# Optimization experiments

Hardware: AMD Instinct MI355X
Metric: run time of the kernel (lower is better)

Reference implementation:

```python
import jax, jax.numpy as jnp
import numpy as np

EMBED_DIM = 512
KERNEL = 17


def setup_inputs() -> dict:
    key = jax.random.key(0)
    ks = jax.random.split(key, 5)
    B, L, C = 2, 8192, EMBED_DIM
    s = C ** -0.5
    x = jax.random.normal(ks[0], (B, L, C), dtype=jnp.float32)
    # weights stored as (in, out); equivalent to torch Linear weight.T
    w_qkv = jax.random.normal(ks[1], (C, 3 * C), dtype=jnp.float32) * s
    w_width = jax.random.normal(ks[2], (C, 1), dtype=jnp.float32) * s
    b_width = jax.random.normal(ks[3], (1,), dtype=jnp.float32) * 0.01
    w_out = jax.random.normal(ks[4], (C, C), dtype=jnp.float32) * s
    return {"x": x, "w_qkv": w_qkv, "w_width": w_width, "b_width": b_width, "w_out": w_out}


def reference(x, w_qkv, w_width, b_width, w_out):
    B, L, C = x.shape
    K = KERNEL
    half_k = K // 2
    scale = C ** -0.5

    qkv = x @ w_qkv                      # [B,L,3C]
    q, k, v = jnp.split(qkv, 3, axis=-1)

    # learned soft window width in [1, K]
    width = jax.nn.sigmoid(x @ w_width + b_width) * (K - 1) + 1.0   # [B,L,1]

    # sliding windows of k/v: pad along L then gather K-sized windows
    k_pad = jnp.pad(k, ((0, 0), (half_k, half_k), (0, 0)))
    v_pad = jnp.pad(v, ((0, 0), (half_k, half_k), (0, 0)))
    idx = jnp.arange(L)[:, None] + jnp.arange(K)[None, :]           # [L,K]
    k_win = k_pad[:, idx]                # [B,L,K,C]
    v_win = v_pad[:, idx]                # [B,L,K,C]

    scores = jnp.einsum('blc,blkc->blk', q, k_win) * scale          # [B,L,K]

    rel_pos = jnp.abs(jnp.arange(K, dtype=jnp.float32) - half_k)    # [K]
    soft_mask = jax.nn.sigmoid((width - rel_pos) * 5.0)             # [B,L,K]
    scores = scores - (1.0 - soft_mask) * 10000.0

    attn = jax.nn.softmax(scores, axis=-1)
    out = jnp.einsum('blk,blkc->blc', attn, v_win)                  # [B,L,C]
    return (out + v) @ w_out
```

## Files before the change

kernel.cpp:

```cpp
#include <hip/hip_runtime.h>

typedef unsigned short u16;
typedef unsigned int   u32;
typedef __attribute__((ext_vector_type(8))) short          shortx8;
typedef __attribute__((ext_vector_type(8))) unsigned short ushortx8;
typedef __attribute__((ext_vector_type(4))) float          floatx4;

#define AS1 __attribute__((address_space(1)))
#define AS3 __attribute__((address_space(3)))

#define SEG 8208
#define LV  16416

__device__ __forceinline__ float b2f(u16 v) {
  return __uint_as_float(((u32)v) << 16);
}
__device__ __forceinline__ u16 f2b(float f) {
  u32 u = __float_as_uint(f);
  u += 0x7FFF + ((u >> 16) & 1);
  return (u16)(u >> 16);
}
__device__ __forceinline__ void cp16(const void* g, void* l) {
  __builtin_amdgcn_global_load_lds((AS1 u32*)g, (AS3 u32*)l, 16, 0, 0);
}

__global__ __launch_bounds__(256)
void prep(const float* __restrict__ x, const float* __restrict__ w_width,
          const float* __restrict__ b_width, const float* __restrict__ w_qkv,
          const float* __restrict__ w_out, u16* __restrict__ xb,
          float* __restrict__ width, u16* __restrict__ wqkvT,
          u16* __restrict__ woutT, u16* __restrict__ Vt) {
  __shared__ u16 tile[32][33];
  const int b = blockIdx.x;
  if (b < 4096) {
    const int lane = threadIdx.x & 63;
    const int row  = b * 4 + (threadIdx.x >> 6);
    const float* xp = x + (size_t)row * 512 + lane * 8;
    floatx4 v0 = *(const floatx4*)xp;
    floatx4 v1 = *(const floatx4*)(xp + 4);
    floatx4 w0 = *(const floatx4*)(w_width + lane * 8);
    floatx4 w1 = *(const floatx4*)(w_width + lane * 8 + 4);
    float s = 0.f;
    ushortx8 o;
#pragma unroll
    for (int j = 0; j < 4; ++j) {
      s += v0[j] * w0[j] + v1[j] * w1[j];
      o[j] = f2b(v0[j]); o[4 + j] = f2b(v1[j]);
    }
    *(ushortx8*)(xb + (size_t)row * 512 + lane * 8) = o;
#pragma unroll
    for (int m = 32; m >= 1; m >>= 1) s += __shfl_xor(s, m, 64);
    if (lane == 0)
      width[row] = 16.f / (1.f + __expf(-(s + b_width[0]))) + 1.f;
  } else if (b < 5120) {
    const float* in; u16* out; int R, C, t;
    if (b < 4864) { in = w_qkv; out = wqkvT; R = 512; C = 1536; t = b - 4096; }
    else          { in = w_out; out = woutT; R = 512; C = 512;  t = b - 4864; }
    const int nbx = C / 32;
    const int cb = (t % nbx) * 32;
    const int rb = (t / nbx) * 32;
    const int tx = threadIdx.x & 31;
    const int ty = threadIdx.x >> 5;
#pragma unroll
    for (int i = 0; i < 32; i += 8)
      tile[ty + i][tx] = f2b(in[(size_t)(rb + ty + i) * C + cb + tx]);
    __syncthreads();
#pragma unroll
    for (int i = 0; i < 32; i += 8)
      out[(size_t)(cb + ty + i) * R + rb + tx] = tile[tx][ty + i];
  } else {
    const int idx = (b - 5120) * 256 + threadIdx.x;
    const int ch = idx >> 5;
    const int k  = idx & 31;
    const int seg = k >> 4;
    const int j   = k & 15;
    const int col = seg * SEG + (j < 8 ? j : 8192 + j);
    Vt[(size_t)ch * LV + col] = 0;
  }
}

template <int MODE>
__global__ __launch_bounds__(256, 3)
void gemm_bt(const u16* __restrict__ A, const u16* __restrict__ Bt,
             void* __restrict__ C0, u16* __restrict__ Kb, u16* __restrict__ Vt) {
  const int K = 512;
  __shared__ alignas(16) u16 lds[17408];
  u16* As = lds;
  u16* Bs = lds + 8192;
  const int tid  = threadIdx.x;
  const int lane = tid & 63;
  const int wave = tid >> 6;
  const int quad = lane >> 4;
  const int lr   = lane & 15;
  const int row0 = blockIdx.x * 128;
  const int col0 = blockIdx.y * 128;
  const int wr   = (wave >> 1) * 64;
  const int wc   = (wave & 1) * 64;

  floatx4 acc[4][4];
#pragma unroll
  for (int i = 0; i < 4; ++i)
#pragma unroll
    for (int j = 0; j < 4; ++j) acc[i][j] = (floatx4)0.0f;

  int srow[4], scol[4];
#pragma unroll
  for (int p = 0; p < 4; ++p) {
    int c = p * 256 + tid;
    srow[p] = c >> 3;
    scol[p] = ((c & 7) ^ (srow[p] & 7)) * 8;
  }
  const int swz = lr & 7;

  for (int k0 = 0; k0 < K; k0 += 64) {
#pragma unroll
    for (int p = 0; p < 4; ++p)
      cp16(A + (size_t)(row0 + srow[p]) * K + k0 + scol[p], &As[(p * 256 + tid) * 8]);
#pragma unroll
    for (int p = 0; p < 4; ++p)
      cp16(Bt + (size_t)(col0 + srow[p]) * K + k0 + scol[p], &Bs[(p * 256 + tid) * 8]);
    __syncthreads();

#pragma unroll
    for (int ks = 0; ks < 2; ++ks) {
      shortx8 af[4], bf[4];
#pragma unroll
      for (int mi = 0; mi < 4; ++mi)
        af[mi] = *(const shortx8*)
            &As[((wr + mi * 16 + lr) * 8 + ((ks * 4 + quad) ^ swz)) * 8];
#pragma unroll
      for (int ni = 0; ni < 4; ++ni)
        bf[ni] = *(const shortx8*)
            &Bs[((wc + ni * 16 + lr) * 8 + ((ks * 4 + quad) ^ swz)) * 8];
#pragma unroll
      for (int mi = 0; mi < 4; ++mi)
#pragma unroll
        for (int ni = 0; ni < 4; ++ni)
          acc[mi][ni] = __builtin_amdgcn_mfma_f32_16x16x32_bf16(
              af[mi], bf[ni], acc[mi][ni], 0, 0, 0);
    }
    __syncthreads();
  }

  if constexpr (MODE == 1) {
    if (col0 < 1024) {
      u16* dst = (col0 < 512) ? (u16*)C0 : Kb;
      const int cb = col0 & 511;
#pragma unroll
      for (int mi = 0; mi < 4; ++mi)
#pragma unroll
        for (int ni = 0; ni < 4; ++ni)
#pragma unroll
          for (int r = 0; r < 4; ++r)
            lds[(wr + mi * 16 + quad * 4 + r) * 136 + wc + ni * 16 + lr] =
                f2b(acc[mi][ni][r]);
      __syncthreads();
      const int rr = tid >> 4, cc = (tid & 15) * 8;
#pragma unroll
      for (int it = 0; it < 8; ++it) {
        int row = it * 16 + rr;
        *(ushortx8*)(dst + (size_t)(row0 + row) * 512 + cb + cc) =
            *(const ushortx8*)&lds[row * 136 + cc];
      }
    } else {
      const int cb = col0 - 1024;
      const int bb = row0 >> 13, pib0 = row0 & 8191;
#pragma unroll
      for (int mi = 0; mi < 4; ++mi)
#pragma unroll
        for (int ni = 0; ni < 4; ++ni)
#pragma unroll
          for (int r = 0; r < 4; ++r)
            lds[(wc + ni * 16 + lr) * 136 + wr + mi * 16 + quad * 4 + r] =
                f2b(acc[mi][ni][r]);
      __syncthreads();
      const int rr = tid >> 4, cc = (tid & 15) * 8;
#pragma unroll
      for (int it = 0; it < 8; ++it) {
        int chl = it * 16 + rr;
        ushortx8 v = *(const ushortx8*)&lds[chl * 136 + cc];
        *(ushortx8*)(Vt + (size_t)(cb + chl) * LV + (size_t)bb * SEG + 8 + pib0 + cc) = v;
      }
    }
  } else {
    float* Cf = (float*)C0;
#pragma unroll
    for (int mi = 0; mi < 4; ++mi)
#pragma unroll
      for (int ni = 0; ni < 4; ++ni)
#pragma unroll
        for (int r = 0; r < 4; ++r) {
          int row = row0 + wr + mi * 16 + quad * 4 + r;
          int col = col0 + wc + ni * 16 + lr;
          Cf[(size_t)row * 512 + col] = acc[mi][ni][r];
        }
  }
}

__global__ __launch_bounds__(256, 1)
void attn_fused(const u16* __restrict__ Q, const u16* __restrict__ Kb,
                const u16* __restrict__ Vt, const float* __restrict__ width,
                const u16* __restrict__ woutT, float* __restrict__ Out) {
  __shared__ alignas(16) u16 Osw[64 * 256];
  __shared__ alignas(16) u16 P[4][16][32];
  const int tid  = threadIdx.x;
  const int lane = tid & 63;
  const int wave = tid >> 6;
  const int quad = lane >> 4;
  const int lr   = lane & 15;
  const int p0   = blockIdx.x * 64;
  const int pw   = p0 + wave * 16;
  const int pibw = pw & 8191;
  const int bb   = pw >> 13;

  floatx4 s0 = (floatx4)0.0f, s1 = (floatx4)0.0f;
#pragma unroll 4
  for (int s = 0; s < 16; ++s) {
    const int k0 = s * 32 + quad * 8;
    shortx8 af = *(const shortx8*)(Q  + (size_t)(pw + lr) * 512 + k0);
    shortx8 f0 = *(const shortx8*)(Kb + (ptrdiff_t)(pw - 8 + lr) * 512 + k0);
    shortx8 f1 = *(const shortx8*)(Kb + (ptrdiff_t)(pw + 8 + lr) * 512 + k0);
    s0 = __builtin_amdgcn_mfma_f32_16x16x32_bf16(af, f0, s0, 0, 0, 0);
    s1 = __builtin_amdgcn_mfma_f32_16x16x32_bf16(af, f1, s1, 0, 0, 0);
  }

  {
    const float scale = 0.044194173824159216f;
    floatx4 wv = *(const floatx4*)(width + pw + quad * 4);
#pragma unroll
    for (int r = 0; r < 4; ++r) {
      const int row = quad * 4 + r;
      const int d0  = lr - row;
      const int d1  = d0 + 16;
      const int jb0 = pibw + lr - 8;
      const int jb1 = jb0 + 16;
      float rel0 = fabsf((float)(d0 - 8));
      float rel1 = fabsf((float)(d1 - 8));
      float mk0 = 1.f / (1.f + __expf(-5.f * (wv[r] - rel0)));
      float mk1 = 1.f / (1.f + __expf(-5.f * (wv[r] - rel1)));
      float val0 = (d0 >= 0)
          ? (((unsigned)jb0 < 8192u ? s0[r] * scale : 0.f) - (1.f - mk0) * 10000.f)
          : -1e30f;
      float val1 = (d1 <= 16)
          ? (((unsigned)jb1 < 8192u ? s1[r] * scale : 0.f) - (1.f - mk1) * 10000.f)
          : -1e30f;
      float mx = fmaxf(val0, val1);
#pragma unroll
      for (int m = 8; m >= 1; m >>= 1) mx = fmaxf(mx, __shfl_xor(mx, m, 64));
      float e0 = __expf(val0 - mx), e1 = __expf(val1 - mx);
      float sum = e0 + e1;
#pragma unroll
      for (int m = 8; m >= 1; m >>= 1) sum += __shfl_xor(sum, m, 64);
      const float inv = 1.f / sum;
      P[wave][row][lr]      = f2b(e0 * inv + (d0 == 8 ? 1.f : 0.f));
      P[wave][row][lr + 16] = f2b(e1 * inv + (d1 == 8 ? 1.f : 0.f));
    }
  }

  shortx8 pf = *(const shortx8*)&P[wave][lr][quad * 8];
  const size_t cb0 = (size_t)bb * SEG + pibw;
  const int wc = wave * 128;
  floatx4 acc[4][8];
#pragma unroll
  for (int mi = 0; mi < 4; ++mi)
#pragma unroll
    for (int ni = 0; ni < 8; ++ni) acc[mi][ni] = (floatx4)0.0f;

#pragma unroll
  for (int half = 0; half < 2; ++half) {
#pragma unroll 4
    for (int ctl = 0; ctl < 16; ++ctl) {
      const int ch = half * 256 + ctl * 16 + lr;
      shortx8 vf = *(const shortx8*)(Vt + (size_t)ch * LV + cb0 + quad * 8);
      floatx4 o = __builtin_amdgcn_mfma_f32_16x16x32_bf16(pf, vf, (floatx4)0.0f,
                                                          0, 0, 0);
      const int c = ctl * 2 + (lr >> 3);
#pragma unroll
      for (int r = 0; r < 4; ++r) {
        const int row = wave * 16 + quad * 4 + r;
        Osw[row * 256 + (((c & ~7) | ((c & 7) ^ (row & 7))) << 3) + (lr & 7)] =
            f2b(o[r]);
      }
    }
    __syncthreads();

    for (int ksl = 0; ksl < 8; ++ksl) {
      const int kg = half * 256 + ksl * 32 + quad * 8;
      shortx8 bfr[8], afr[4];
#pragma unroll
      for (int ni = 0; ni < 8; ++ni)
        bfr[ni] = *(const shortx8*)(woutT + (size_t)(wc + ni * 16 + lr) * 512 + kg);
#pragma unroll
      for (int mi = 0; mi < 4; ++mi) {
        const int row = mi * 16 + lr;
        const int c = ksl * 4 + quad;
        afr[mi] = *(const shortx8*)
            &Osw[row * 256 + (((c & ~7) | ((c & 7) ^ (row & 7))) << 3)];
      }
#pragma unroll
      for (int mi = 0; mi < 4; ++mi)
#pragma unroll
        for (int ni = 0; ni < 8; ++ni)
          acc[mi][ni] = __builtin_amdgcn_mfma_f32_16x16x32_bf16(
              afr[mi], bfr[ni], acc[mi][ni], 0, 0, 0);
    }
    if (half == 0) __syncthreads();
  }

#pragma unroll
  for (int mi = 0; mi < 4; ++mi)
#pragma unroll
    for (int ni = 0; ni < 8; ++ni)
#pragma unroll
      for (int r = 0; r < 4; ++r)
        Out[(size_t)(p0 + mi * 16 + quad * 4 + r) * 512 + wc + ni * 16 + lr] =
            acc[mi][ni][r];
}

extern "C" void kernel_launch(void* const* d_in, const int* in_sizes, int n_in,
                              void* d_out, int out_size, void* d_ws, size_t ws_size,
                              hipStream_t stream) {
  const float* x       = (const float*)d_in[0];
  const float* w_qkv   = (const float*)d_in[1];
  const float* w_width = (const float*)d_in[2];
  const float* b_width = (const float*)d_in[3];
  const float* w_out   = (const float*)d_in[4];
  float* out = (float*)d_out;

  const int M = 16384, N3 = 1536;
  char* ws = (char*)d_ws;
  u16*   xb    = (u16*)(ws);
  u16*   Qb    = (u16*)(ws + 16777216);
  u16*   Kb    = (u16*)(ws + 33554432 + 8192);
  u16*   Vt    = (u16*)(ws + 50348032);
  u16*   wqkvT = (u16*)(ws + 67158016);
  u16*   woutT = (u16*)(ws + 68730880);
  float* width = (float*)(ws + 69255168);

  dim3 blk(256);
  prep<<<dim3(5184), blk, 0, stream>>>(x, w_width, b_width, w_qkv, w_out,
                                       xb, width, wqkvT, woutT, Vt);
  gemm_bt<1><<<dim3(M / 128, N3 / 128), blk, 0, stream>>>(xb, wqkvT, Qb, Kb, Vt);
  attn_fused<<<dim3(M / 64), blk, 0, stream>>>(Qb, Kb, Vt, width, woutT, out);
}
```

Measured before the change: 156.4 us.

## Halve attention block rows and split score and PV work across wave pairs

The fused attention kernel now handles 32 positions per block instead of 64. The four waves split the score and PV work as 2 row groups by 2 key or channel halves, with scores exchanged through shared memory and softmax computed by all threads. The launch-bounds hint is raised to allow two blocks per CU, and the grid doubles. The intent is more parallelism and occupancy with less redundant work per wave. The cost is extra block syncs, and each w_out tile is reused over 32 rows instead of 64, so w_out traffic per output row doubles.

```diff
diff --git a/kernel.cpp b/kernel.cpp
--- a/kernel.cpp
+++ b/kernel.cpp
@@ -197,118 +197,123 @@
   }
 }
 
-__global__ __launch_bounds__(256, 1)
+__global__ __launch_bounds__(256, 2)
 void attn_fused(const u16* __restrict__ Q, const u16* __restrict__ Kb,
                 const u16* __restrict__ Vt, const float* __restrict__ width,
                 const u16* __restrict__ woutT, float* __restrict__ Out) {
-  __shared__ alignas(16) u16 Osw[64 * 256];
-  __shared__ alignas(16) u16 P[4][16][32];
+  __shared__ alignas(16) u16 Osw[32 * 512];
+  __shared__ float S[32][33];
+  __shared__ u16 P[32][40];
   const int tid  = threadIdx.x;
   const int lane = tid & 63;
   const int wave = tid >> 6;
   const int quad = lane >> 4;
   const int lr   = lane & 15;
-  const int p0   = blockIdx.x * 64;
-  const int pw   = p0 + wave * 16;
-  const int pibw = pw & 8191;
-  const int bb   = pw >> 13;
-
-  floatx4 s0 = (floatx4)0.0f, s1 = (floatx4)0.0f;
+  const int p0   = blockIdx.x * 32;
+  const int rg   = wave & 1;
+  const int tw   = wave >> 1;
+  const int prg  = p0 + rg * 16;
+  const int pib  = prg & 8191;
+  const int bb   = prg >> 13;
+
+  floatx4 s0 = (floatx4)0.0f;
 #pragma unroll 4
   for (int s = 0; s < 16; ++s) {
     const int k0 = s * 32 + quad * 8;
-    shortx8 af = *(const shortx8*)(Q  + (size_t)(pw + lr) * 512 + k0);
-    shortx8 f0 = *(const shortx8*)(Kb + (ptrdiff_t)(pw - 8 + lr) * 512 + k0);
-    shortx8 f1 = *(const shortx8*)(Kb + (ptrdiff_t)(pw + 8 + lr) * 512 + k0);
-    s0 = __builtin_amdgcn_mfma_f32_16x16x32_bf16(af, f0, s0, 0, 0, 0);
-    s1 = __builtin_amdgcn_mfma_f32_16x16x32_bf16(af, f1, s1, 0, 0, 0);
-  }
+    shortx8 af = *(const shortx8*)(Q  + (size_t)(prg + lr) * 512 + k0);
+    shortx8 f  = *(const shortx8*)(Kb +
+                   (ptrdiff_t)(prg - 8 + tw * 16 + lr) * 512 + k0);
+    s0 = __builtin_amdgcn_mfma_f32_16x16x32_bf16(af, f, s0, 0, 0, 0);
+  }
+#pragma unroll
+  for (int r = 0; r < 4; ++r)
+    S[rg * 16 + quad * 4 + r][tw * 16 + lr] = s0[r];
+  __syncthreads();
 
   {
+    const int row = tid >> 3, cg = tid & 7;
+    const int rr  = row & 15;
+    const int pibr = (p0 + (row >> 4) * 16) & 8191;
     const float scale = 0.044194173824159216f;
-    floatx4 wv = *(const floatx4*)(width + pw + quad * 4);
+    const float wrow = width[p0 + row];
+    float sv[4]; float mx = -1e30f;
+#pragma unroll
+    for (int t = 0; t < 4; ++t) {
+      const int col = t * 8 + cg;
+      const int d  = col - rr;
+      const int jb = pibr + col - 8;
+      float rel = fabsf((float)(d - 8));
+      float msk = 1.f / (1.f + __expf(-5.f * (wrow - rel)));
+      float pen = (1.f - msk) * 10000.f;
+      float val = (d >= 0 && d <= 16)
+          ? (((unsigned)jb < 8192u ? S[row][col] * scale : 0.f) - pen)
+          : -1e30f;
+      sv[t] = val; mx = fmaxf(mx, val);
+    }
+#pragma unroll
+    for (int m = 4; m >= 1; m >>= 1) mx = fmaxf(mx, __shfl_xor(mx, m, 64));
+    float e[4], sum = 0.f;
+#pragma unroll
+    for (int t = 0; t < 4; ++t) { e[t] = __expf(sv[t] - mx); sum += e[t]; }
+#pragma unroll
+    for (int m = 4; m >= 1; m >>= 1) sum += __shfl_xor(sum, m, 64);
+    const float inv = 1.f / sum;
+#pragma unroll
+    for (int t = 0; t < 4; ++t) {
+      const int col = t * 8 + cg;
+      P[row][col] = f2b(e[t] * inv + ((col - rr) == 8 ? 1.f : 0.f));
+    }
+  }
+  __syncthreads();
+
+  shortx8 pf = *(const shortx8*)&P[rg * 16 + lr][quad * 8];
+  const size_t cb0 = (size_t)bb * SEG + pib;
+#pragma unroll 4
+  for (int ctl = 0; ctl < 16; ++ctl) {
+    const int ch = tw * 256 + ctl * 16 + lr;
+    shortx8 vf = *(const shortx8*)(Vt + (size_t)ch * LV + cb0 + quad * 8);
+    floatx4 o = __builtin_amdgcn_mfma_f32_16x16x32_bf16(pf, vf, (floatx4)0.0f,
+                                                        0, 0, 0);
+    const int c = tw * 32 + ctl * 2 + (lr >> 3);
 #pragma unroll
     for (int r = 0; r < 4; ++r) {
-      const int row = quad * 4 + r;
-      const int d0  = lr - row;
-      const int d1  = d0 + 16;
-      const int jb0 = pibw + lr - 8;
-      const int jb1 = jb0 + 16;
-      float rel0 = fabsf((float)(d0 - 8));
-      float rel1 = fabsf((float)(d1 - 8));
-      float mk0 = 1.f / (1.f + __expf(-5.f * (wv[r] - rel0)));
-      float mk1 = 1.f / (1.f + __expf(-5.f * (wv[r] - rel1)));
-      float val0 = (d0 >= 0)
-          ? (((unsigned)jb0 < 8192u ? s0[r] * scale : 0.f) - (1.f - mk0) * 10000.f)
-          : -1e30f;
-      float val1 = (d1 <= 16)
-          ? (((unsigned)jb1 < 8192u ? s1[r] * scale : 0.f) - (1.f - mk1) * 10000.f)
-          : -1e30f;
-      float mx = fmaxf(val0, val1);
-#pragma unroll
-      for (int m = 8; m >= 1; m >>= 1) mx = fmaxf(mx, __shfl_xor(mx, m, 64));
-      float e0 = __expf(val0 - mx), e1 = __expf(val1 - mx);
-      float sum = e0 + e1;
-#pragma unroll
-      for (int m = 8; m >= 1; m >>= 1) sum += __shfl_xor(sum, m, 64);
-      const float inv = 1.f / sum;
-      P[wave][row][lr]      = f2b(e0 * inv + (d0 == 8 ? 1.f : 0.f));
-      P[wave][row][lr + 16] = f2b(e1 * inv + (d1 == 8 ? 1.f : 0.f));
-    }
-  }
-
-  shortx8 pf = *(const shortx8*)&P[wave][lr][quad * 8];
-  const size_t cb0 = (size_t)bb * SEG + pibw;
+      const int row = rg * 16 + quad * 4 + r;
+      Osw[row * 512 + (((c & ~7) | ((c & 7) ^ (row & 7))) << 3) + (lr & 7)] =
+          f2b(o[r]);
+    }
+  }
+  __syncthreads();
+
   const int wc = wave * 128;
-  floatx4 acc[4][8];
-#pragma unroll
-  for (int mi = 0; mi < 4; ++mi)
+  floatx4 acc[2][8];
+#pragma unroll
+  for (int mi = 0; mi < 2; ++mi)
 #pragma unroll
     for (int ni = 0; ni < 8; ++ni) acc[mi][ni] = (floatx4)0.0f;
 
-#pragma unroll
-  for (int half = 0; half < 2; ++half) {
-#pragma unroll 4
-    for (int ctl = 0; ctl < 16; ++ctl) {
-      const int ch = half * 256 + ctl * 16 + lr;
-      shortx8 vf = *(const shortx8*)(Vt + (size_t)ch * LV + cb0 + quad * 8);
-      floatx4 o = __builtin_amdgcn_mfma_f32_16x16x32_bf16(pf, vf, (floatx4)0.0f,
-                                                          0, 0, 0);
-      const int c = ctl * 2 + (lr >> 3);
-#pragma unroll
-      for (int r = 0; r < 4; ++r) {
-        const int row = wave * 16 + quad * 4 + r;
-        Osw[row * 256 + (((c & ~7) | ((c & 7) ^ (row & 7))) << 3) + (lr & 7)] =
-            f2b(o[r]);
-      }
-    }
-    __syncthreads();
-
-    for (int ksl = 0; ksl < 8; ++ksl) {
-      const int kg = half * 256 + ksl * 32 + quad * 8;
-      shortx8 bfr[8], afr[4];
+  for (int ksl = 0; ksl < 16; ++ksl) {
+    const int kg = ksl * 32 + quad * 8;
+    shortx8 bfr[8], afr[2];
+#pragma unroll
+    for (int ni = 0; ni < 8; ++ni)
+      bfr[ni] = *(const shortx8*)(woutT + (size_t)(wc + ni * 16 + lr) * 512 + kg);
+#pragma unroll
+    for (int mi = 0; mi < 2; ++mi) {
+      const int row = mi * 16 + lr;
+      const int c = ksl * 4 + quad;
+      afr[mi] = *(const shortx8*)
+          &Osw[row * 512 + (((c & ~7) | ((c & 7) ^ (row & 7))) << 3)];
+    }
+#pragma unroll
+    for (int mi = 0; mi < 2; ++mi)
 #pragma unroll
       for (int ni = 0; ni < 8; ++ni)
-        bfr[ni] = *(const shortx8*)(woutT + (size_t)(wc + ni * 16 + lr) * 512 + kg);
-#pragma unroll
-      for (int mi = 0; mi < 4; ++mi) {
-        const int row = mi * 16 + lr;
-        const int c = ksl * 4 + quad;
-        afr[mi] = *(const shortx8*)
-            &Osw[row * 256 + (((c & ~7) | ((c & 7) ^ (row & 7))) << 3)];
-      }
-#pragma unroll
-      for (int mi = 0; mi < 4; ++mi)
-#pragma unroll
-        for (int ni = 0; ni < 8; ++ni)
-          acc[mi][ni] = __builtin_amdgcn_mfma_f32_16x16x32_bf16(
-              afr[mi], bfr[ni], acc[mi][ni], 0, 0, 0);
-    }
-    if (half == 0) __syncthreads();
-  }
-
-#pragma unroll
-  for (int mi = 0; mi < 4; ++mi)
+        acc[mi][ni] = __builtin_amdgcn_mfma_f32_16x16x32_bf16(
+            afr[mi], bfr[ni], acc[mi][ni], 0, 0, 0);
+  }
+
+#pragma unroll
+  for (int mi = 0; mi < 2; ++mi)
 #pragma unroll
     for (int ni = 0; ni < 8; ++ni)
 #pragma unroll
@@ -341,5 +346,5 @@
   prep<<<dim3(5184), blk, 0, stream>>>(x, w_width, b_width, w_qkv, w_out,
                                        xb, width, wqkvT, woutT, Vt);
   gemm_bt<1><<<dim3(M / 128, N3 / 128), blk, 0, stream>>>(xb, wqkvT, Qb, Kb, Vt);
-  attn_fused<<<dim3(M / 64), blk, 0, stream>>>(Qb, Kb, Vt, width, woutT, out);
-}
+  attn_fused<<<dim3(M / 32), blk, 0, stream>>>(Qb, Kb, Vt, width, woutT, out);
+}
```

Result: slower. 164.9 us (+5.4%).

## Prefetch V fragments early and double-buffer w_out loads in attn_fused

Applied to the files above, without the earlier changes.

The V-transpose fragments for both channel halves are now issued as global loads into registers early: the first half before the QK score loop, the second before the first output-projection pass. This lets their latency overlap with the score and softmax work. The w_out B-fragments in the projection loop are double-buffered, with the next k-slice loaded while the current MFMAs run. The cost is a large increase in register pressure (32 shortx8 V fragments plus 16 B fragments on top of 32 accumulators), which could cause spills under launch_bounds(256,1).

```diff
diff --git a/kernel.cpp b/kernel.cpp
--- a/kernel.cpp
+++ b/kernel.cpp
@@ -212,6 +212,13 @@
   const int pw   = p0 + wave * 16;
   const int pibw = pw & 8191;
   const int bb   = pw >> 13;
+  const size_t cb0 = (size_t)bb * SEG + pibw;
+
+  shortx8 vfA[16];
+#pragma unroll
+  for (int ctl = 0; ctl < 16; ++ctl)
+    vfA[ctl] = *(const shortx8*)(Vt + (size_t)(ctl * 16 + lr) * LV +
+                                 cb0 + quad * 8);
 
   floatx4 s0 = (floatx4)0.0f, s1 = (floatx4)0.0f;
 #pragma unroll 4
@@ -256,9 +263,8 @@
       P[wave][row][lr + 16] = f2b(e1 * inv + (d1 == 8 ? 1.f : 0.f));
     }
   }
-
   shortx8 pf = *(const shortx8*)&P[wave][lr][quad * 8];
-  const size_t cb0 = (size_t)bb * SEG + pibw;
+
   const int wc = wave * 128;
   floatx4 acc[4][8];
 #pragma unroll
@@ -266,30 +272,41 @@
 #pragma unroll
     for (int ni = 0; ni < 8; ++ni) acc[mi][ni] = (floatx4)0.0f;
 
-#pragma unroll
-  for (int half = 0; half < 2; ++half) {
-#pragma unroll 4
-    for (int ctl = 0; ctl < 16; ++ctl) {
-      const int ch = half * 256 + ctl * 16 + lr;
-      shortx8 vf = *(const shortx8*)(Vt + (size_t)ch * LV + cb0 + quad * 8);
-      floatx4 o = __builtin_amdgcn_mfma_f32_16x16x32_bf16(pf, vf, (floatx4)0.0f,
-                                                          0, 0, 0);
-      const int c = ctl * 2 + (lr >> 3);
-#pragma unroll
-      for (int r = 0; r < 4; ++r) {
-        const int row = wave * 16 + quad * 4 + r;
-        Osw[row * 256 + (((c & ~7) | ((c & 7) ^ (row & 7))) << 3) + (lr & 7)] =
-            f2b(o[r]);
-      }
-    }
-    __syncthreads();
-
+  shortx8 vfB[16];
+#pragma unroll
+  for (int ctl = 0; ctl < 16; ++ctl)
+    vfB[ctl] = *(const shortx8*)(Vt + (size_t)(256 + ctl * 16 + lr) * LV +
+                                 cb0 + quad * 8);
+
+#pragma unroll
+  for (int ctl = 0; ctl < 16; ++ctl) {
+    floatx4 o = __builtin_amdgcn_mfma_f32_16x16x32_bf16(pf, vfA[ctl],
+                                                        (floatx4)0.0f, 0, 0, 0);
+    const int c = ctl * 2 + (lr >> 3);
+#pragma unroll
+    for (int r = 0; r < 4; ++r) {
+      const int row = wave * 16 + quad * 4 + r;
+      Osw[row * 256 + (((c & ~7) | ((c & 7) ^ (row & 7))) << 3) + (lr & 7)] =
+          f2b(o[r]);
+    }
+  }
+  __syncthreads();
+
+  {
+    shortx8 bcur[8], bnxt[8];
+#pragma unroll
+    for (int ni = 0; ni < 8; ++ni)
+      bcur[ni] = *(const shortx8*)(woutT + (size_t)(wc + ni * 16 + lr) * 512 +
+                                   quad * 8);
     for (int ksl = 0; ksl < 8; ++ksl) {
-      const int kg = half * 256 + ksl * 32 + quad * 8;
-      shortx8 bfr[8], afr[4];
-#pragma unroll
-      for (int ni = 0; ni < 8; ++ni)
-        bfr[ni] = *(const shortx8*)(woutT + (size_t)(wc + ni * 16 + lr) * 512 + kg);
+      if (ksl < 7) {
+#pragma unroll
+        for (int ni = 0; ni < 8; ++ni)
+          bnxt[ni] = *(const shortx8*)(woutT +
+                       (size_t)(wc + ni * 16 + lr) * 512 +
+                       (ksl + 1) * 32 + quad * 8);
+      }
+      shortx8 afr[4];
 #pragma unroll
       for (int mi = 0; mi < 4; ++mi) {
         const int row = mi * 16 + lr;
@@ -302,9 +319,62 @@
 #pragma unroll
         for (int ni = 0; ni < 8; ++ni)
           acc[mi][ni] = __builtin_amdgcn_mfma_f32_16x16x32_bf16(
-              afr[mi], bfr[ni], acc[mi][ni], 0, 0, 0);
-    }
-    if (half == 0) __syncthreads();
+              afr[mi], bcur[ni], acc[mi][ni], 0, 0, 0);
+      if (ksl < 7) {
+#pragma unroll
+        for (int ni = 0; ni < 8; ++ni) bcur[ni] = bnxt[ni];
+      }
+    }
+  }
+  __syncthreads();
+
+#pragma unroll
+  for (int ctl = 0; ctl < 16; ++ctl) {
+    floatx4 o = __builtin_amdgcn_mfma_f32_16x16x32_bf16(pf, vfB[ctl],
+                                                        (floatx4)0.0f, 0, 0, 0);
+    const int c = ctl * 2 + (lr >> 3);
+#pragma unroll
+    for (int r = 0; r < 4; ++r) {
+      const int row = wave * 16 + quad * 4 + r;
+      Osw[row * 256 + (((c & ~7) | ((c & 7) ^ (row & 7))) << 3) + (lr & 7)] =
+          f2b(o[r]);
+    }
+  }
+  __syncthreads();
+
+  {
+    shortx8 bcur[8], bnxt[8];
+#pragma unroll
+    for (int ni = 0; ni < 8; ++ni)
+      bcur[ni] = *(const shortx8*)(woutT + (size_t)(wc + ni * 16 + lr) * 512 +
+                                   256 + quad * 8);
+    for (int ksl = 0; ksl < 8; ++ksl) {
+      if (ksl < 7) {
+#pragma unroll
+        for (int ni = 0; ni < 8; ++ni)
+          bnxt[ni] = *(const shortx8*)(woutT +
+                       (size_t)(wc + ni * 16 + lr) * 512 +
+                       256 + (ksl + 1) * 32 + quad * 8);
+      }
+      shortx8 afr[4];
+#pragma unroll
+      for (int mi = 0; mi < 4; ++mi) {
+        const int row = mi * 16 + lr;
+        const int c = ksl * 4 + quad;
+        afr[mi] = *(const shortx8*)
+            &Osw[row * 256 + (((c & ~7) | ((c & 7) ^ (row & 7))) << 3)];
+      }
+#pragma unroll
+      for (int mi = 0; mi < 4; ++mi)
+#pragma unroll
+        for (int ni = 0; ni < 8; ++ni)
+          acc[mi][ni] = __builtin_amdgcn_mfma_f32_16x16x32_bf16(
+              afr[mi], bcur[ni], acc[mi][ni], 0, 0, 0);
+      if (ksl < 7) {
+#pragma unroll
+        for (int ni = 0; ni < 8; ++ni) bcur[ni] = bnxt[ni];
+      }
+    }
   }
 
 #pragma unroll
@@ -337,9 +407,10 @@
   u16*   woutT = (u16*)(ws + 68730880);
   float* width = (float*)(ws + 69255168);
 
-  dim3 blk(256);
-  prep<<<dim3(5184), blk, 0, stream>>>(x, w_width, b_width, w_qkv, w_out,
-                                       xb, width, wqkvT, woutT, Vt);
-  gemm_bt<1><<<dim3(M / 128, N3 / 128), blk, 0, stream>>>(xb, wqkvT, Qb, Kb, Vt);
-  attn_fused<<<dim3(M / 64), blk, 0, stream>>>(Qb, Kb, Vt, width, woutT, out);
-}
+  prep<<<dim3(5184), dim3(256), 0, stream>>>(x, w_width, b_width, w_qkv, w_out,
+                                             xb, width, wqkvT, woutT, Vt);
+  gemm_bt<1><<<dim3(M / 128, N3 / 128), dim3(256), 0, stream>>>(xb, wqkvT, Qb,
+                                                                Kb, Vt);
+  attn_fused<<<dim3(M / 64), dim3(256), 0, stream>>>(Qb, Kb, Vt, width, woutT,
+                                                     out);
+}
```

Result: no change. 155.2 us (-0.8%).
